# Performance work log

Hardware: AMD Instinct MI355X
Metric: run time of the kernel (lower is better)

## Reference

```python
import jax, jax.numpy as jnp
import numpy as np

EPS = 1e-5

def _conv1x1(x, W, b):
    # x: [B,Ci,H,W], W: [Co,Ci]
    return jnp.einsum('oi,bihw->bohw', W, x) + b[None, :, None, None]

def _bn(x, gamma, beta, mean, var):
    # inference-mode BatchNorm2d
    s = gamma / jnp.sqrt(var + EPS)
    return x * s[None, :, None, None] + (beta - mean * s)[None, :, None, None]

def _conv3x3(x, W, b):
    y = jax.lax.conv_general_dilated(x, W, (1, 1), 'SAME',
                                     dimension_numbers=('NCHW', 'OIHW', 'NCHW'))
    return y + b[None, :, None, None]

def _sparsemax_last(S):
    # sparsemax over the last axis (TrackHSPA: max-subtract, sort, cumsum, threshold)
    S = S - jnp.max(S, axis=-1, keepdims=True)
    srt = -jnp.sort(-S, axis=-1)                 # descending sort
    csum = jnp.cumsum(srt, axis=-1) - 1.0
    N = S.shape[-1]
    ar = jnp.arange(1, N + 1, dtype=S.dtype)
    mask = ar * srt > csum
    k = jnp.sum(mask, axis=-1, keepdims=True)    # support size per row
    tau = jnp.take_along_axis(csum, k - 1, axis=-1) / k.astype(S.dtype)
    return jnp.maximum(S - tau, 0.0)

def _forward(zf, xf, Wq, bq, Ws, bs, Wg, bg, g_gamma, g_beta, g_mean, g_var,
             Wfi, bfi, fi_gamma, fi_beta, fi_mean, fi_var,
             Wm, bm, m_gamma, m_beta, m_mean, m_var, prelu_a):
    B, C, Hx, Wx = xf.shape
    # ---- Graph_Attention_Union (cross-attention) ----
    xf_t = _conv1x1(xf, Wq, bq).reshape(B, C, -1)      # [B,C,Nx]
    zf_t = _conv1x1(zf, Ws, bs).reshape(B, C, -1)      # [B,C,Nz]
    xf_g = jax.nn.relu(_bn(_conv1x1(xf, Wg, bg), g_gamma, g_beta, g_mean, g_var))
    zf_g = jax.nn.relu(_bn(_conv1x1(zf, Wg, bg), g_gamma, g_beta, g_mean, g_var))
    sim = jnp.einsum('bcn,bcm->bnm', xf_t, zf_t)       # [B,Nx,Nz]
    attn = jax.nn.softmax(sim, axis=2)
    emb = jnp.einsum('bcm,bnm->bcn', zf_g.reshape(B, C, -1), attn)
    emb = emb.reshape(B, C, Hx, Wx)
    gat = jax.nn.relu(_bn(_conv1x1(jnp.concatenate([emb, xf_g], axis=1), Wfi, bfi),
                          fi_gamma, fi_beta, fi_mean, fi_var))
    # ---- TrackHSPA (adaptive sparsemax self-attention) ----
    e = _conv3x3(gat, Wm, bm)
    e = _bn(e, m_gamma, m_beta, m_mean, m_var)
    e = jnp.where(e >= 0, e, prelu_a * e)              # PReLU (single param)
    N = Hx * Wx
    ef = e.reshape(B, -1, N)                           # [B,C',N]
    S = jnp.einsum('bdi,bdj->bij', ef, ef)             # [B,N,N]
    P = _sparsemax_last(S)
    out = jnp.einsum('bcn,bnm->bcm', gat.reshape(B, C, N), P)
    return out.reshape(B, C, Hx, Wx) + gat


def setup_inputs():
    key = jax.random.key(0)
    ks = jax.random.split(key, 8)
    B, C, Hz, Wz, Hx, Wx = 32, 256, 7, 7, 31, 31
    Cm = C // 4
    f = lambda k, shape: jax.random.normal(k, shape, jnp.float32) * 0.05
    return {
        'zf': jax.random.normal(ks[0], (B, C, Hz, Wz), jnp.float32),
        'xf': jax.random.normal(ks[1], (B, C, Hx, Wx), jnp.float32),
        'Wq': f(ks[2], (C, C)), 'bq': jnp.zeros((C,), jnp.float32),
        'Ws': f(ks[3], (C, C)), 'bs': jnp.zeros((C,), jnp.float32),
        'Wg': f(ks[4], (C, C)), 'bg': jnp.zeros((C,), jnp.float32),
        'g_gamma': jnp.ones((C,), jnp.float32), 'g_beta': jnp.zeros((C,), jnp.float32),
        'g_mean': jnp.zeros((C,), jnp.float32), 'g_var': jnp.ones((C,), jnp.float32),
        'Wfi': f(ks[5], (C, 2 * C)), 'bfi': jnp.zeros((C,), jnp.float32),
        'fi_gamma': jnp.ones((C,), jnp.float32), 'fi_beta': jnp.zeros((C,), jnp.float32),
        'fi_mean': jnp.zeros((C,), jnp.float32), 'fi_var': jnp.ones((C,), jnp.float32),
        'Wm': f(ks[6], (Cm, C, 3, 3)), 'bm': jnp.zeros((Cm,), jnp.float32),
        'm_gamma': jnp.ones((Cm,), jnp.float32), 'm_beta': jnp.zeros((Cm,), jnp.float32),
        'm_mean': jnp.zeros((Cm,), jnp.float32), 'm_var': jnp.ones((Cm,), jnp.float32),
        'prelu_a': jnp.array(0.25, jnp.float32),
    }


def reference(zf, xf, Wq, bq, Ws, bs, Wg, bg, g_gamma, g_beta, g_mean, g_var,
              Wfi, bfi, fi_gamma, fi_beta, fi_mean, fi_var,
              Wm, bm, m_gamma, m_beta, m_mean, m_var, prelu_a):
    return _forward(zf, xf, Wq, bq, Ws, bs, Wg, bg, g_gamma, g_beta, g_mean, g_var,
                    Wfi, bfi, fi_gamma, fi_beta, fi_mean, fi_var,
                    Wm, bm, m_gamma, m_beta, m_mean, m_var, prelu_a)
```

## Files before the change

### kernel.cpp

```cpp
#include <hip/hip_runtime.h>
#include <cstdint>
#include <cstddef>
#include <math.h>

typedef __attribute__((ext_vector_type(8))) short short8;
typedef __attribute__((ext_vector_type(4))) float floatx4;
typedef unsigned short ushort_t;

__device__ __forceinline__ ushort_t f2bf(float x) {
    union { float f; unsigned u; } v; v.f = x;
    unsigned r = v.u + 0x7FFF + ((v.u >> 16) & 1);
    return (ushort_t)(r >> 16);
}
__device__ __forceinline__ float bf2f(ushort_t h) {
    union { unsigned u; float f; } v; v.u = ((unsigned)h) << 16; return v.f;
}
__device__ __forceinline__ void split2(float v, ushort_t& h, ushort_t& l) {
    h = f2bf(v);
    l = f2bf(v - bf2f(h));
}

#define MFMA(a, b, c) __builtin_amdgcn_mfma_f32_16x16x32_bf16((a), (b), (c), 0, 0, 0)

__device__ __forceinline__ void gload_lds16(const void* g, void* l) {
    __builtin_amdgcn_global_load_lds(
        (const __attribute__((address_space(1))) unsigned*)g,
        (__attribute__((address_space(3))) unsigned*)l, 16, 0, 0);
}

__global__ void prep_all_kernel(
    const float* __restrict__ Wq, const float* __restrict__ Ws,
    const float* __restrict__ Wg, const float* __restrict__ Wfi,
    const float* __restrict__ Wm,
    const float* bq, const float* bs,
    const float* bg, const float* gg, const float* gb, const float* gm, const float* gv,
    const float* bfi, const float* fg, const float* fb, const float* fm, const float* fv,
    const float* bm, const float* mg, const float* mb, const float* mm, const float* mv,
    ushort_t* Wq_h, ushort_t* Wq_l, ushort_t* Ws_h, ushort_t* Ws_l,
    ushort_t* Wg_h, ushort_t* Wg_l, ushort_t* Wfi_h, ushort_t* Wfi_l,
    ushort_t* wm_h, ushort_t* wm_l, float* scsh)
{
    int bid = blockIdx.x, t = threadIdx.x;
    if (bid < 256) {
        int i = bid * 256 + t; ushort_t h, l; split2(Wq[i], h, l); Wq_h[i] = h; Wq_l[i] = l;
    } else if (bid < 512) {
        int i = (bid - 256) * 256 + t; ushort_t h, l; split2(Ws[i], h, l); Ws_h[i] = h; Ws_l[i] = l;
    } else if (bid < 768) {
        int i = (bid - 512) * 256 + t; ushort_t h, l; split2(Wg[i], h, l); Wg_h[i] = h; Wg_l[i] = l;
    } else if (bid < 1280) {
        int i = (bid - 768) * 256 + t; ushort_t h, l; split2(Wfi[i], h, l); Wfi_h[i] = h; Wfi_l[i] = l;
    } else if (bid < 1856) {
        int i = (bid - 1280) * 256 + t;
        int c = i & 255, m = (i >> 8) & 63, tap = i >> 14;
        ushort_t h, l; split2(Wm[((size_t)m * 256 + c) * 9 + tap], h, l);
        wm_h[i] = h; wm_l[i] = l;
    } else {
        if (t < 256) {
            scsh[t] = 1.f;        scsh[256 + t] = bq[t];
            scsh[512 + t] = 1.f;  scsh[768 + t] = bs[t];
            float s = gg[t] * rsqrtf(gv[t] + 1e-5f);
            scsh[1024 + t] = s;   scsh[1280 + t] = gb[t] + s * (bg[t] - gm[t]);
            float s2 = fg[t] * rsqrtf(fv[t] + 1e-5f);
            scsh[1536 + t] = s2;  scsh[1792 + t] = fb[t] + s2 * (bfi[t] - fm[t]);
            if (t < 64) {
                float s3 = mg[t] * rsqrtf(mv[t] + 1e-5f);
                scsh[2048 + t] = s3; scsh[2112 + t] = mb[t] + s3 * (bm[t] - mm[t]);
            }
        }
    }
}

__global__ void halo_zero_kernel(ushort_t* __restrict__ gxh, ushort_t* __restrict__ gxl) {
    int i = blockIdx.x * 256 + threadIdx.x;
    int b = i >> 7, k = i & 127;
    int r;
    if (k < 33) r = k;
    else if (k < 66) r = 32 * 33 + (k - 33);
    else { int k2 = k - 66; r = ((k2 >> 1) + 1) * 33 + ((k2 & 1) ? 32 : 0); }
    uint4* ph = (uint4*)(gxh + ((size_t)b * 1089 + r) * 256);
    uint4* pl = (uint4*)(gxl + ((size_t)b * 1089 + r) * 256);
    uint4 z = make_uint4(0, 0, 0, 0);
#pragma unroll
    for (int s = 0; s < 32; s++) { ph[s] = z; pl[s] = z; }
}

__global__ __launch_bounds__(256) void transpose_in_kernel(
    const float* __restrict__ in, ushort_t* __restrict__ oh, ushort_t* __restrict__ ol,
    int Nsrc, int Npad)
{
    int b = blockIdx.z;
    const float* ib = in + (size_t)b * 256 * Nsrc;
    ushort_t* obh = oh + (size_t)b * Npad * 256;
    ushort_t* obl = ol + (size_t)b * Npad * 256;
    __shared__ float tile[32][33];
    int n0 = blockIdx.x * 32, c0 = blockIdx.y * 32;
    int tx = threadIdx.x & 31, ty = threadIdx.x >> 5;
#pragma unroll
    for (int r = 0; r < 4; r++) {
        int c = c0 + ty + r * 8, n = n0 + tx;
        tile[ty + r * 8][tx] = (n < Nsrc) ? ib[(size_t)c * Nsrc + n] : 0.f;
    }
    __syncthreads();
#pragma unroll
    for (int r = 0; r < 4; r++) {
        int n = n0 + ty + r * 8, c = c0 + tx;
        if (n < Nsrc) {
            ushort_t h, l; split2(tile[tx][ty + r * 8], h, l);
            obh[(size_t)n * 256 + c] = h;
            obl[(size_t)n * 256 + c] = l;
        }
    }
}

__global__ __launch_bounds__(256, 4) void dualconv_mfma_kernel(
    const ushort_t* __restrict__ Xh, const ushort_t* __restrict__ Xl,
    const ushort_t* __restrict__ W1h, const ushort_t* __restrict__ W1l,
    const ushort_t* __restrict__ W2h, const ushort_t* __restrict__ W2l,
    const float* __restrict__ sc1, const float* __restrict__ sh1,
    const float* __restrict__ sc2, const float* __restrict__ sh2,
    int relu1, int relu2,
    ushort_t* __restrict__ O1h, ushort_t* __restrict__ O1l,
    ushort_t* __restrict__ O2h, ushort_t* __restrict__ O2l,
    ushort_t* __restrict__ O2ch, ushort_t* __restrict__ O2cl, int cpitch,
    int K, int Nvalid, int NpadIn, int NpadOut)
{
    __shared__ ushort_t Bs[16384];
    int b = blockIdx.x;
    int half = blockIdx.y & 1;
    int n0 = (blockIdx.y >> 1) * 32;
    const ushort_t* Xbh = Xh + (size_t)b * NpadIn * K;
    const ushort_t* Xbl = Xl + (size_t)b * NpadIn * K;
    int tid = threadIdx.x, w = tid >> 6, l = tid & 63, lc = l & 15, q = l >> 4;
    int m0 = w * 64;

#pragma unroll
    for (int r = 0; r < 8; r++) {
        int d = r * 4096 + w * 1024 + l * 16;
        int seg = d >> 14;
        int dr = d & 16383;
        int row = dr >> 9;
        int inrow = (dr & 511) ^ ((row & 7) << 4);
        int srow = n0 + row; if (srow > NpadIn - 1) srow = NpadIn - 1;
        const ushort_t* src = (seg ? Xbl : Xbh) + (size_t)srow * K + (inrow >> 1);
        char* dst = (char*)Bs + (r * 4096 + w * 1024);
        gload_lds16(src, dst);
    }
    __syncthreads();

    const ushort_t* Wh = half ? W2h : W1h;
    const ushort_t* Wl = half ? W2l : W1l;
    const float* sc = half ? sc2 : sc1;
    const float* sh = half ? sh2 : sh1;
    int relu = half ? relu2 : relu1;
    ushort_t* Obh = (half ? O2h : O1h) + (size_t)b * NpadOut * 256;
    ushort_t* Obl = (half ? O2l : O1l) + (size_t)b * NpadOut * 256;

#define DC_LOADA(K0, AH, AL) do { \
    _Pragma("unroll") \
    for (int mt_ = 0; mt_ < 4; mt_++) { \
        size_t off_ = (size_t)(m0 + mt_ * 16 + lc) * K + (K0) + q * 8; \
        AH[mt_] = *(const short8*)(Wh + off_); \
        AL[mt_] = *(const short8*)(Wl + off_); \
    } \
} while (0)
#define DC_LDSB(K0, BH, BL) do { \
    _Pragma("unroll") \
    for (int jt_ = 0; jt_ < 2; jt_++) { \
        int row_ = jt_ * 16 + lc; \
        int koff_ = (((K0) + q * 8) * 2) ^ ((row_ & 7) << 4); \
        BH[jt_] = *(const short8*)((const char*)Bs + row_ * 512 + koff_); \
        BL[jt_] = *(const short8*)((const char*)Bs + 16384 + row_ * 512 + koff_); \
    } \
} while (0)
#define DC_MFMA(AH, AL, BH, BL) do { \
    _Pragma("unroll") \
    for (int mt_ = 0; mt_ < 4; mt_++) \
    _Pragma("unroll") \
    for (int jt_ = 0; jt_ < 2; jt_++) { \
        acc[mt_][jt_] = MFMA(AH[mt_], BH[jt_], acc[mt_][jt_]); \
        acc[mt_][jt_] = MFMA(AH[mt_], BL[jt_], acc[mt_][jt_]); \
        acc[mt_][jt_] = MFMA(AL[mt_], BH[jt_], acc[mt_][jt_]); \
    } \
} while (0)

    floatx4 acc[4][2];
#pragma unroll
    for (int i = 0; i < 4; i++)
#pragma unroll
        for (int j = 0; j < 2; j++) acc[i][j] = (floatx4){0.f, 0.f, 0.f, 0.f};

    {
        short8 ah0[4], al0[4], ah1[4], al1[4], bh[2], bl[2];
        DC_LOADA(0, ah0, al0);
        for (int k0 = 0; k0 < K; k0 += 64) {
            DC_LOADA(k0 + 32, ah1, al1);
            DC_LDSB(k0, bh, bl);
            DC_MFMA(ah0, al0, bh, bl);
            if (k0 + 64 < K) DC_LOADA(k0 + 64, ah0, al0);
            DC_LDSB(k0 + 32, bh, bl);
            DC_MFMA(ah1, al1, bh, bl);
        }
    }
#undef DC_LOADA
#undef DC_LDSB
#undef DC_MFMA

#pragma unroll
    for (int mt = 0; mt < 4; mt++) {
        int mb = m0 + mt * 16 + q * 4;
        float s0 = sc[mb], s1 = sc[mb + 1], s2 = sc[mb + 2], s3 = sc[mb + 3];
        float h0 = sh[mb], h1 = sh[mb + 1], h2 = sh[mb + 2], h3 = sh[mb + 3];
#pragma unroll
        for (int jt = 0; jt < 2; jt++) {
            int n = n0 + jt * 16 + lc;
            if (n >= Nvalid) continue;
            float v0 = acc[mt][jt][0] * s0 + h0;
            float v1 = acc[mt][jt][1] * s1 + h1;
            float v2 = acc[mt][jt][2] * s2 + h2;
            float v3 = acc[mt][jt][3] * s3 + h3;
            if (relu) { v0 = fmaxf(v0, 0.f); v1 = fmaxf(v1, 0.f); v2 = fmaxf(v2, 0.f); v3 = fmaxf(v3, 0.f); }
            ushort_t e0, f0, e1, f1, e2, f2, e3, f3;
            split2(v0, e0, f0); split2(v1, e1, f1); split2(v2, e2, f2); split2(v3, e3, f3);
            *(ushort4*)(Obh + (size_t)n * 256 + mb) = make_ushort4(e0, e1, e2, e3);
            *(ushort4*)(Obl + (size_t)n * 256 + mb) = make_ushort4(f0, f1, f2, f3);
            if (half && O2ch) {
                O2ch[((size_t)b * 256 + mb + 0) * cpitch + n] = e0;
                O2ch[((size_t)b * 256 + mb + 1) * cpitch + n] = e1;
                O2ch[((size_t)b * 256 + mb + 2) * cpitch + n] = e2;
                O2ch[((size_t)b * 256 + mb + 3) * cpitch + n] = e3;
                O2cl[((size_t)b * 256 + mb + 0) * cpitch + n] = f0;
                O2cl[((size_t)b * 256 + mb + 1) * cpitch + n] = f1;
                O2cl[((size_t)b * 256 + mb + 2) * cpitch + n] = f2;
                O2cl[((size_t)b * 256 + mb + 3) * cpitch + n] = f3;
            }
        }
    }
}

__global__ __launch_bounds__(256) void attn_mfma_kernel(
    const ushort_t* __restrict__ xth, const ushort_t* __restrict__ xtl,
    const ushort_t* __restrict__ zth, const ushort_t* __restrict__ ztl,
    const ushort_t* __restrict__ zgh, const ushort_t* __restrict__ zgl,
    ushort_t* __restrict__ eh, ushort_t* __restrict__ el)
{
    __shared__ float S[64][68];
    __shared__ ushort_t awh[64][72], awl[64][72];
    __shared__ float T[4][16][20];
    int b = blockIdx.x, n0 = blockIdx.y * 64;
    int tid = threadIdx.x, w = tid >> 6, l = tid & 63, lc = l & 15, q = l >> 4;
    const ushort_t* xhb = xth + (size_t)b * 992 * 256;
    const ushort_t* xlb = xtl + (size_t)b * 992 * 256;
    const ushort_t* zhb = zth + (size_t)b * 64 * 256;
    const ushort_t* zlb = ztl + (size_t)b * 64 * 256;
    const ushort_t* ghb = zgh + (size_t)b * 256 * 64;
    const ushort_t* glb = zgl + (size_t)b * 256 * 64;

    int rowg = n0 + w * 16 + lc;
#pragma unroll
    for (int ct = 0; ct < 4; ct++) {
        floatx4 acc = (floatx4){0.f, 0.f, 0.f, 0.f};
        for (int k0 = 0; k0 < 256; k0 += 32) {
            short8 ah = *(const short8*)(xhb + (size_t)rowg * 256 + k0 + q * 8);
            short8 al = *(const short8*)(xlb + (size_t)rowg * 256 + k0 + q * 8);
            short8 bh = *(const short8*)(zhb + (size_t)(ct * 16 + lc) * 256 + k0 + q * 8);
            short8 bl = *(const short8*)(zlb + (size_t)(ct * 16 + lc) * 256 + k0 + q * 8);
            acc = MFMA(ah, bh, acc);
            acc = MFMA(ah, bl, acc);
            acc = MFMA(al, bh, acc);
        }
#pragma unroll
        for (int r = 0; r < 4; r++) S[w * 16 + q * 4 + r][ct * 16 + lc] = acc[r];
    }
    __syncthreads();
    if (tid < 64) {
        float mx = -INFINITY;
        for (int m = 0; m < 49; m++) mx = fmaxf(mx, S[tid][m]);
        float sum = 0.f;
        for (int m = 0; m < 49; m++) { float e = __expf(S[tid][m] - mx); S[tid][m] = e; sum += e; }
        float inv = 1.f / sum;
        for (int m = 0; m < 64; m++) {
            float vv = (m < 49) ? S[tid][m] * inv : 0.f;
            ushort_t hh, ll; split2(vv, hh, ll);
            awh[tid][m] = hh; awl[tid][m] = ll;
        }
    }
    __syncthreads();
    int nw = l >> 2, cg = l & 3;
#pragma unroll
    for (int ct = 0; ct < 16; ct++) {
        floatx4 acc = (floatx4){0.f, 0.f, 0.f, 0.f};
#pragma unroll
        for (int k0 = 0; k0 < 64; k0 += 32) {
            short8 ah = *(const short8*)(&awh[w * 16 + lc][k0 + q * 8]);
            short8 al = *(const short8*)(&awl[w * 16 + lc][k0 + q * 8]);
            short8 bh = *(const short8*)(ghb + (size_t)(ct * 16 + lc) * 64 + k0 + q * 8);
            short8 bl = *(const short8*)(glb + (size_t)(ct * 16 + lc) * 64 + k0 + q * 8);
            acc = MFMA(ah, bh, acc);
            acc = MFMA(ah, bl, acc);
            acc = MFMA(al, bh, acc);
        }
#pragma unroll
        for (int r = 0; r < 4; r++) T[w][q * 4 + r][lc] = acc[r];
        float4 vv = *(const float4*)&T[w][nw][cg * 4];
        int n = n0 + w * 16 + nw;
        if (n < 961) {
            ushort_t h0, l0, h1, l1, h2, l2_, h3, l3;
            split2(vv.x, h0, l0); split2(vv.y, h1, l1);
            split2(vv.z, h2, l2_); split2(vv.w, h3, l3);
            size_t off = ((size_t)b * 992 + n) * 256 + ct * 16 + cg * 4;
            *(ushort4*)(eh + off) = make_ushort4(h0, h1, h2, h3);
            *(ushort4*)(el + off) = make_ushort4(l0, l1, l2_, l3);
        }
    }
}

__global__ __launch_bounds__(256, 2) void fi_mfma_kernel(
    const ushort_t* __restrict__ Eh, const ushort_t* __restrict__ El,
    const ushort_t* __restrict__ Gh, const ushort_t* __restrict__ Gl,
    const ushort_t* __restrict__ Wh, const ushort_t* __restrict__ Wl,
    const float* __restrict__ sc, const float* __restrict__ sh,
    ushort_t* __restrict__ gxh, ushort_t* __restrict__ gxl,
    ushort_t* __restrict__ gat_nf)
{
    __shared__ ushort_t Bs[16384];
    int b = blockIdx.x;
    const ushort_t* Ebh = Eh + (size_t)b * 992 * 256;
    const ushort_t* Ebl = El + (size_t)b * 992 * 256;
    const ushort_t* Gbh = Gh + (size_t)b * 992 * 256;
    const ushort_t* Gbl = Gl + (size_t)b * 992 * 256;
    ushort_t* gxhb = gxh + (size_t)b * 1089 * 256;
    ushort_t* gxlb = gxl + (size_t)b * 1089 * 256;
    ushort_t* gn = gat_nf + (size_t)b * 256 * 992;
    int tid = threadIdx.x, w = tid >> 6, l = tid & 63, lc = l & 15, q = l >> 4;
    int m0 = w * 64, nb0 = blockIdx.y * 32;

    floatx4 acc[4][2];
#pragma unroll
    for (int i = 0; i < 4; i++)
#pragma unroll
        for (int j = 0; j < 2; j++) acc[i][j] = (floatx4){0.f, 0.f, 0.f, 0.f};

#define FI_LOADA(K0, AH, AL) do { \
    _Pragma("unroll") \
    for (int mt_ = 0; mt_ < 4; mt_++) { \
        size_t off_ = (size_t)(m0 + mt_ * 16 + lc) * 512 + (K0) + q * 8; \
        AH[mt_] = *(const short8*)(Wh + off_); \
        AL[mt_] = *(const short8*)(Wl + off_); \
    } \
} while (0)
#define FI_LDSB(K0, BH, BL) do { \
    _Pragma("unroll") \
    for (int jt_ = 0; jt_ < 2; jt_++) { \
        int row_ = jt_ * 16 + lc; \
        int koff_ = (((K0) + q * 8) * 2) ^ ((row_ & 7) << 4); \
        BH[jt_] = *(const short8*)((const char*)Bs + row_ * 512 + koff_); \
        BL[jt_] = *(const short8*)((const char*)Bs + 16384 + row_ * 512 + koff_); \
    } \
} while (0)
#define FI_MFMA(AH, AL, BH, BL) do { \
    _Pragma("unroll") \
    for (int mt_ = 0; mt_ < 4; mt_++) \
    _Pragma("unroll") \
    for (int jt_ = 0; jt_ < 2; jt_++) { \
        acc[mt_][jt_] = MFMA(AH[mt_], BH[jt_], acc[mt_][jt_]); \
        acc[mt_][jt_] = MFMA(AH[mt_], BL[jt_], acc[mt_][jt_]); \
        acc[mt_][jt_] = MFMA(AL[mt_], BH[jt_], acc[mt_][jt_]); \
    } \
} while (0)

    for (int p = 0; p < 2; p++) {
        const ushort_t* srcH = p ? Gbh : Ebh;
        const ushort_t* srcL = p ? Gbl : Ebl;
        if (p) __syncthreads();
#pragma unroll
        for (int r = 0; r < 8; r++) {
            int d = r * 4096 + w * 1024 + l * 16;
            int seg = d >> 14;
            int dr = d & 16383;
            int row = dr >> 9;
            int inrow = (dr & 511) ^ ((row & 7) << 4);
            int srow = nb0 + row; if (srow > 991) srow = 991;
            const ushort_t* src = (seg ? srcL : srcH) + (size_t)srow * 256 + (inrow >> 1);
            char* dst = (char*)Bs + (r * 4096 + w * 1024);
            gload_lds16(src, dst);
        }
        __syncthreads();

        int pb = p * 256;
        short8 ah0[4], al0[4], ah1[4], al1[4], bh[2], bl[2];
        FI_LOADA(pb, ah0, al0);
        for (int kk = 0; kk < 256; kk += 64) {
            FI_LOADA(pb + kk + 32, ah1, al1);
            FI_LDSB(kk, bh, bl);
            FI_MFMA(ah0, al0, bh, bl);
            if (kk + 64 < 256) FI_LOADA(pb + kk + 64, ah0, al0);
            FI_LDSB(kk + 32, bh, bl);
            FI_MFMA(ah1, al1, bh, bl);
        }
    }
#undef FI_LOADA
#undef FI_LDSB
#undef FI_MFMA

#pragma unroll
    for (int mt = 0; mt < 4; mt++) {
        int mb = m0 + mt * 16 + q * 4;
        float s0 = sc[mb], s1 = sc[mb + 1], s2 = sc[mb + 2], s3 = sc[mb + 3];
        float h0 = sh[mb], h1 = sh[mb + 1], h2 = sh[mb + 2], h3 = sh[mb + 3];
#pragma unroll
        for (int jt = 0; jt < 2; jt++) {
            int n = nb0 + jt * 16 + lc;
            if (n >= 961) continue;
            float v0 = fmaxf(acc[mt][jt][0] * s0 + h0, 0.f);
            float v1 = fmaxf(acc[mt][jt][1] * s1 + h1, 0.f);
            float v2 = fmaxf(acc[mt][jt][2] * s2 + h2, 0.f);
            float v3 = fmaxf(acc[mt][jt][3] * s3 + h3, 0.f);
            ushort_t a0, b0, a1, b1, a2, b2, a3, b3;
            split2(v0, a0, b0); split2(v1, a1, b1); split2(v2, a2, b2); split2(v3, a3, b3);
            int hh = n / 31, ww2 = n - hh * 31;
            int row = (hh + 1) * 33 + (ww2 + 1);
            *(ushort4*)(gxhb + (size_t)row * 256 + mb) = make_ushort4(a0, a1, a2, a3);
            *(ushort4*)(gxlb + (size_t)row * 256 + mb) = make_ushort4(b0, b1, b2, b3);
            gn[(size_t)(mb + 0) * 992 + n] = a0;
            gn[(size_t)(mb + 1) * 992 + n] = a1;
            gn[(size_t)(mb + 2) * 992 + n] = a2;
            gn[(size_t)(mb + 3) * 992 + n] = a3;
        }
    }
}

__global__ __launch_bounds__(256, 2) void conv3x3_mfma_kernel(
    const ushort_t* __restrict__ gxh, const ushort_t* __restrict__ gxl,
    const ushort_t* __restrict__ wmh, const ushort_t* __restrict__ wml,
    const float* __restrict__ sc, const float* __restrict__ sh,
    const float* __restrict__ prelu_a,
    ushort_t* __restrict__ eh, ushort_t* __restrict__ el)
{
    __shared__ float Sp[4][2048];
    int b = blockIdx.x;
    const ushort_t* gxhb = gxh + (size_t)b * 1089 * 256;
    const ushort_t* gxlb = gxl + (size_t)b * 1089 * 256;
    ushort_t* ebh = eh + (size_t)b * 1024 * 64;
    ushort_t* ebl = el + (size_t)b * 1024 * 64;
    int tid = threadIdx.x, w = tid >> 6, l = tid & 63, lc = l & 15, q = l >> 4;
    int j0 = blockIdx.y * 64;

    int base[4];
#pragma unroll
    for (int jt = 0; jt < 4; jt++) {
        int j = j0 + jt * 16 + lc; if (j > 960) j = 960;
        int hh = j / 31, ww2 = j - hh * 31;
        base[jt] = (hh + 1) * 33 + (ww2 + 1);
    }

    floatx4 acc[4][4];
#pragma unroll
    for (int i = 0; i < 4; i++)
#pragma unroll
        for (int j = 0; j < 4; j++) acc[i][j] = (floatx4){0.f, 0.f, 0.f, 0.f};

#define C3_LOAD(SL, AH, AL, BH, BL) do { \
    int sl_ = (SL); \
    int tap_ = (sl_ >= 9) ? sl_ - 9 : sl_; \
    int k0_ = (w * 2 + ((sl_ >= 9) ? 1 : 0)) * 32; \
    int doff_ = (tap_ / 3 - 1) * 33 + (tap_ % 3 - 1); \
    const ushort_t* wth_ = wmh + tap_ * 16384; \
    const ushort_t* wtl_ = wml + tap_ * 16384; \
    _Pragma("unroll") \
    for (int mt_ = 0; mt_ < 4; mt_++) { \
        size_t off_ = (size_t)(mt_ * 16 + lc) * 256 + k0_ + q * 8; \
        AH[mt_] = *(const short8*)(wth_ + off_); \
        AL[mt_] = *(const short8*)(wtl_ + off_); \
    } \
    _Pragma("unroll") \
    for (int jt_ = 0; jt_ < 4; jt_++) { \
        size_t off_ = (size_t)(base[jt_] + doff_) * 256 + k0_ + q * 8; \
        BH[jt_] = *(const short8*)(gxhb + off_); \
        BL[jt_] = *(const short8*)(gxlb + off_); \
    } \
} while (0)
#define C3_MFMA(AH, AL, BH, BL) do { \
    _Pragma("unroll") \
    for (int mt_ = 0; mt_ < 4; mt_++) \
    _Pragma("unroll") \
    for (int jt_ = 0; jt_ < 4; jt_++) { \
        acc[mt_][jt_] = MFMA(AH[mt_], BH[jt_], acc[mt_][jt_]); \
        acc[mt_][jt_] = MFMA(AH[mt_], BL[jt_], acc[mt_][jt_]); \
        acc[mt_][jt_] = MFMA(AL[mt_], BH[jt_], acc[mt_][jt_]); \
    } \
} while (0)

    short8 A0h[4], A0l[4], B0h[4], B0l[4];
    short8 A1h[4], A1l[4], B1h[4], B1l[4];
    C3_LOAD(0, A0h, A0l, B0h, B0l);
#pragma unroll
    for (int it = 0; it < 9; it++) {
        C3_LOAD(it * 2 + 1, A1h, A1l, B1h, B1l);
        C3_MFMA(A0h, A0l, B0h, B0l);
        if (it < 8) C3_LOAD(it * 2 + 2, A0h, A0l, B0h, B0l);
        C3_MFMA(A1h, A1l, B1h, B1l);
    }
#undef C3_LOAD
#undef C3_MFMA

    float pa = prelu_a[0];
#pragma unroll
    for (int ph = 0; ph < 2; ph++) {
        __syncthreads();
#pragma unroll
        for (int mt = 0; mt < 4; mt++)
#pragma unroll
            for (int jt = 0; jt < 2; jt++)
#pragma unroll
                for (int r = 0; r < 4; r++)
                    Sp[w][(mt * 16 + q * 4 + r) * 32 + jt * 16 + lc] = acc[mt][ph * 2 + jt][r];
        __syncthreads();
#pragma unroll
        for (int gi = 0; gi < 2; gi++) {
            int g = tid + gi * 256;
            int j = g & 31, mg = g >> 5;
            int m = mg * 4;
            int jj = j0 + ph * 32 + j;
            if (jj >= 961) continue;
            float v[4];
#pragma unroll
            for (int i = 0; i < 4; i++) {
                int idx = (m + i) * 32 + j;
                v[i] = Sp[0][idx] + Sp[1][idx] + Sp[2][idx] + Sp[3][idx];
                v[i] = v[i] * sc[m + i] + sh[m + i];
                v[i] = v[i] >= 0.f ? v[i] : pa * v[i];
            }
            ushort_t a0, b0, a1, b1, a2, b2, a3, b3;
            split2(v[0], a0, b0); split2(v[1], a1, b1);
            split2(v[2], a2, b2); split2(v[3], a3, b3);
            *(ushort4*)(ebh + (size_t)jj * 64 + m) = make_ushort4(a0, a1, a2, a3);
            *(ushort4*)(ebl + (size_t)jj * 64 + m) = make_ushort4(b0, b1, b2, b3);
        }
    }
}

__global__ __launch_bounds__(512) void hspa_mfma_kernel(
    const ushort_t* __restrict__ eh, const ushort_t* __restrict__ el,
    ushort_t* __restrict__ PT)
{
    const int PITCH = 978;
    __shared__ float S[16 * 978];
    int b = blockIdx.x, nb = blockIdx.y;
    const ushort_t* ebh = eh + (size_t)b * 1024 * 64;
    const ushort_t* ebl = el + (size_t)b * 1024 * 64;
    ushort_t* Pb = PT + (size_t)b * 1024 * 992;
    int tid = threadIdx.x, w = tid >> 6, l = tid & 63, lc = l & 15, q = l >> 4;
    int n0 = nb * 32;

    short8 Ah[2][2], Al[2][2];
#pragma unroll
    for (int g = 0; g < 2; g++)
#pragma unroll
        for (int kh = 0; kh < 2; kh++) {
            size_t off = (size_t)(n0 + g * 16 + lc) * 64 + kh * 32 + q * 8;
            Ah[g][kh] = *(const short8*)(ebh + off);
            Al[g][kh] = *(const short8*)(ebl + off);
        }

    floatx4 acc[2][8];
#pragma unroll
    for (int g = 0; g < 2; g++)
#pragma unroll
        for (int s = 0; s < 8; s++) acc[g][s] = (floatx4){0.f, 0.f, 0.f, 0.f};

#define HS_LOADB(SLOT, BH0, BL0, BH1, BL1) do { \
    int jt_ = w + (SLOT) * 8; if (jt_ > 60) jt_ = 60; \
    size_t o_ = (size_t)(jt_ * 16 + lc) * 64 + q * 8; \
    BH0 = *(const short8*)(ebh + o_); \
    BL0 = *(const short8*)(ebl + o_); \
    BH1 = *(const short8*)(ebh + o_ + 32); \
    BL1 = *(const short8*)(ebl + o_ + 32); \
} while (0)

    {
        short8 b0h[2], b0l[2], b1h[2], b1l[2];
        HS_LOADB(0, b0h[0], b0l[0], b1h[0], b1l[0]);
#pragma unroll
        for (int s = 0; s < 8; s++) {
            const int cur = s & 1, nxt = cur ^ 1;
            if (s < 7) HS_LOADB(s + 1, b0h[nxt], b0l[nxt], b1h[nxt], b1l[nxt]);
#pragma unroll
            for (int g = 0; g < 2; g++) {
                floatx4 a = acc[g][s];
                a = MFMA(Ah[g][0], b0h[cur], a);
                a = MFMA(Ah[g][0], b0l[cur], a);
                a = MFMA(Al[g][0], b0h[cur], a);
                a = MFMA(Ah[g][1], b1h[cur], a);
                a = MFMA(Ah[g][1], b1l[cur], a);
                a = MFMA(Al[g][1], b1h[cur], a);
                acc[g][s] = a;
            }
        }
    }
#undef HS_LOADB

#pragma unroll
    for (int g = 0; g < 2; g++) {
        if (g) __syncthreads();
#pragma unroll
        for (int s = 0; s < 8; s++) {
            int jt = w + s * 8;
            if (jt < 61) {
                int j = jt * 16 + lc;
#pragma unroll
                for (int r = 0; r < 4; r++)
                    S[(q * 4 + r) * PITCH + j] = acc[g][s][r];
            }
        }
        __syncthreads();

        int r0 = w * 2, r1 = w * 2 + 1;
        float sv0[16], sv1[16];
        float mx0 = -INFINITY, mx1 = -INFINITY;
#pragma unroll
        for (int t = 0; t < 16; t++) {
            int j = l + t * 64;
            float s0 = (j < 961) ? S[r0 * PITCH + j] : -INFINITY;
            float s1 = (j < 961) ? S[r1 * PITCH + j] : -INFINITY;
            sv0[t] = s0; sv1[t] = s1;
            mx0 = fmaxf(mx0, s0); mx1 = fmaxf(mx1, s1);
        }
        for (int off = 32; off; off >>= 1) {
            mx0 = fmaxf(mx0, __shfl_xor(mx0, off));
            mx1 = fmaxf(mx1, __shfl_xor(mx1, off));
        }
#pragma unroll
        for (int t = 0; t < 16; t++) { sv0[t] -= mx0; sv1[t] -= mx1; }

        float tau0 = -1.f, tau1 = -1.f;
        for (int it = 0; it < 16; it++) {
            float s0 = 0.f, c0 = 0.f, s1 = 0.f, c1 = 0.f;
#pragma unroll
            for (int t = 0; t < 16; t++) {
                if (sv0[t] > tau0) { s0 += sv0[t]; c0 += 1.f; }
                if (sv1[t] > tau1) { s1 += sv1[t]; c1 += 1.f; }
            }
            for (int off = 32; off; off >>= 1) {
                s0 += __shfl_xor(s0, off); c0 += __shfl_xor(c0, off);
                s1 += __shfl_xor(s1, off); c1 += __shfl_xor(c1, off);
            }
            float nt0 = (s0 - 1.f) / c0;
            float nt1 = (s1 - 1.f) / c1;
            bool conv = (nt0 == tau0) && (nt1 == tau1);
            tau0 = nt0; tau1 = nt1;
            if (conv) break;
        }
#pragma unroll
        for (int t = 0; t < 16; t++) {
            int j = l + t * 64;
            if (j < 976) {
                S[r0 * PITCH + j] = (j < 961) ? fmaxf(sv0[t] - tau0, 0.f) : 0.f;
                S[r1 * PITCH + j] = (j < 961) ? fmaxf(sv1[t] - tau1, 0.f) : 0.f;
            }
        }
        __syncthreads();

        int nbase = n0 + g * 16;
        if (nbase < 976) {
            for (int j = tid; j < 976; j += 512) {
                union { ushort_t u[8]; uint4 v; } p0, p1;
#pragma unroll
                for (int r = 0; r < 8; r++)  p0.u[r] = f2bf(S[r * PITCH + j]);
#pragma unroll
                for (int r = 0; r < 8; r++)  p1.u[r] = f2bf(S[(8 + r) * PITCH + j]);
                ushort_t* dst = Pb + (size_t)j * 992 + nbase;
                *(uint4*)(dst) = p0.v;
                *(uint4*)(dst + 8) = p1.v;
            }
        }
    }
}

__global__ __launch_bounds__(256, 2) void out_mfma_kernel(
    const ushort_t* __restrict__ gat_nf, const ushort_t* __restrict__ PT,
    float* __restrict__ out)
{
    int b = blockIdx.x, jb = blockIdx.y;
    const ushort_t* gb = gat_nf + (size_t)b * 256 * 992;
    const ushort_t* Pb = PT + (size_t)b * 1024 * 992;
    float* ob = out + (size_t)b * 256 * 961;
    int tid = threadIdx.x, w = tid >> 6, l = tid & 63, lc = l & 15, q = l >> 4;
    int m0 = w * 64, j0 = jb * 64;

    floatx4 acc[4][4];
#pragma unroll
    for (int i = 0; i < 4; i++)
#pragma unroll
        for (int j = 0; j < 4; j++) acc[i][j] = (floatx4){0.f, 0.f, 0.f, 0.f};

#define OUT_LOAD(K0, AA, BB) do { \
    _Pragma("unroll") \
    for (int mt_ = 0; mt_ < 4; mt_++) \
        AA[mt_] = *(const short8*)(gb + (size_t)(m0 + mt_ * 16 + lc) * 992 + (K0) + q * 8); \
    _Pragma("unroll") \
    for (int jt_ = 0; jt_ < 4; jt_++) \
        BB[jt_] = *(const short8*)(Pb + (size_t)(j0 + jt_ * 16 + lc) * 992 + (K0) + q * 8); \
} while (0)
#define OUT_MFMA(AA, BB) do { \
    _Pragma("unroll") \
    for (int mt_ = 0; mt_ < 4; mt_++) \
    _Pragma("unroll") \
    for (int jt_ = 0; jt_ < 4; jt_++) \
        acc[mt_][jt_] = MFMA(AA[mt_], BB[jt_], acc[mt_][jt_]); \
} while (0)

    short8 a0[4], b0[4], a1[4], b1[4];
    OUT_LOAD(0, a0, b0);
    for (int k0 = 0; k0 < 960; k0 += 64) {
        OUT_LOAD(k0 + 32, a1, b1);
        OUT_MFMA(a0, b0);
        OUT_LOAD(k0 + 64, a0, b0);
        OUT_MFMA(a1, b1);
    }
    OUT_MFMA(a0, b0);
#undef OUT_LOAD
#undef OUT_MFMA

#pragma unroll
    for (int mt = 0; mt < 4; mt++) {
        int mb = m0 + mt * 16 + q * 4;
#pragma unroll
        for (int jt = 0; jt < 4; jt++) {
            int j = j0 + jt * 16 + lc;
            if (j >= 961) continue;
#pragma unroll
            for (int r = 0; r < 4; r++) {
                float g = bf2f(gb[(size_t)(mb + r) * 992 + j]);
                ob[(size_t)(mb + r) * 961 + j] = acc[mt][jt][r] + g;
            }
        }
    }
}

extern "C" void kernel_launch(void* const* d_in, const int* in_sizes, int n_in,
                              void* d_out, int out_size, void* d_ws, size_t ws_size,
                              hipStream_t stream)
{
    const float* zf      = (const float*)d_in[0];
    const float* xf      = (const float*)d_in[1];
    const float* Wq      = (const float*)d_in[2];
    const float* bq      = (const float*)d_in[3];
    const float* Ws      = (const float*)d_in[4];
    const float* bs      = (const float*)d_in[5];
    const float* Wg      = (const float*)d_in[6];
    const float* bg      = (const float*)d_in[7];
    const float* g_gamma = (const float*)d_in[8];
    const float* g_beta  = (const float*)d_in[9];
    const float* g_mean  = (const float*)d_in[10];
    const float* g_var   = (const float*)d_in[11];
    const float* Wfi     = (const float*)d_in[12];
    const float* bfi     = (const float*)d_in[13];
    const float* fi_gamma= (const float*)d_in[14];
    const float* fi_beta = (const float*)d_in[15];
    const float* fi_mean = (const float*)d_in[16];
    const float* fi_var  = (const float*)d_in[17];
    const float* Wm      = (const float*)d_in[18];
    const float* bm      = (const float*)d_in[19];
    const float* m_gamma = (const float*)d_in[20];
    const float* m_beta  = (const float*)d_in[21];
    const float* m_mean  = (const float*)d_in[22];
    const float* m_var   = (const float*)d_in[23];
    const float* prelu_a = (const float*)d_in[24];
    float* out = (float*)d_out;

    ushort_t* ws = (ushort_t*)d_ws;
    ushort_t* Wq_h  = ws + 0;         ushort_t* Wq_l  = ws + 65536;
    ushort_t* Ws_h  = ws + 131072;    ushort_t* Ws_l  = ws + 196608;
    ushort_t* Wg_h  = ws + 262144;    ushort_t* Wg_l  = ws + 327680;
    ushort_t* Wfi_h = ws + 393216;    ushort_t* Wfi_l = ws + 524288;
    ushort_t* wm_h  = ws + 655360;    ushort_t* wm_l  = ws + 802816;
    ushort_t* XT_h    = ws + 950272;
    ushort_t* XT_l    = ws + 9076736;
    ushort_t* xf_tT_h = ws + 17203200;
    ushort_t* xf_tT_l = ws + 25329664;
    ushort_t* zf_tT_h = ws + 33456128;
    ushort_t* zf_tT_l = ws + 33980416;
    ushort_t* zf_gT_h = ws + 34504704;
    ushort_t* zf_gT_l = ws + 35028992;
    ushort_t* xf_gT_h = ws + 35553280;
    ushort_t* xf_gT_l = ws + 43679744;
    ushort_t* gat_nf  = ws + 51806208;
    ushort_t* eT_h    = ws + 59932672;
    ushort_t* eT_l    = ws + 62029824;
    ushort_t* PT      = ws + 64126976;
    ushort_t* gxT_h   = ws + 64126976;
    ushort_t* gxT_l   = ws + 73048064;
    ushort_t* embT_h  = XT_h;
    ushort_t* embT_l  = XT_l;
    ushort_t* zfT_h   = ws + 96632832;
    ushort_t* zfT_l   = ws + 97157120;
    float* scsh       = (float*)(ws + 97681408);
    ushort_t* zgC_h   = ws + 97685760;
    ushort_t* zgC_l   = ws + 98210048;

    const float* sc_q  = scsh + 0,    *sh_q  = scsh + 256;
    const float* sc_s  = scsh + 512,  *sh_s  = scsh + 768;
    const float* sc_g  = scsh + 1024, *sh_g  = scsh + 1280;
    const float* sc_fi = scsh + 1536, *sh_fi = scsh + 1792;
    const float* sc_m  = scsh + 2048, *sh_m  = scsh + 2112;

    prep_all_kernel<<<1857, 256, 0, stream>>>(
        Wq, Ws, Wg, Wfi, Wm,
        bq, bs, bg, g_gamma, g_beta, g_mean, g_var,
        bfi, fi_gamma, fi_beta, fi_mean, fi_var,
        bm, m_gamma, m_beta, m_mean, m_var,
        Wq_h, Wq_l, Ws_h, Ws_l, Wg_h, Wg_l, Wfi_h, Wfi_l, wm_h, wm_l, scsh);

    transpose_in_kernel<<<dim3(31, 8, 32), 256, 0, stream>>>(xf, XT_h, XT_l, 961, 992);
    transpose_in_kernel<<<dim3(2, 8, 32), 256, 0, stream>>>(zf, zfT_h, zfT_l, 49, 64);

    dualconv_mfma_kernel<<<dim3(32, 62), 256, 0, stream>>>(
        XT_h, XT_l, Wq_h, Wq_l, Wg_h, Wg_l,
        sc_q, sh_q, sc_g, sh_g, 0, 1,
        xf_tT_h, xf_tT_l, xf_gT_h, xf_gT_l,
        nullptr, nullptr, 0, 256, 961, 992, 992);
    dualconv_mfma_kernel<<<dim3(32, 4), 256, 0, stream>>>(
        zfT_h, zfT_l, Ws_h, Ws_l, Wg_h, Wg_l,
        sc_s, sh_s, sc_g, sh_g, 0, 1,
        zf_tT_h, zf_tT_l, zf_gT_h, zf_gT_l,
        zgC_h, zgC_l, 64, 256, 49, 64, 64);

    attn_mfma_kernel<<<dim3(32, 16), 256, 0, stream>>>(
        xf_tT_h, xf_tT_l, zf_tT_h, zf_tT_l, zgC_h, zgC_l, embT_h, embT_l);

    halo_zero_kernel<<<16, 256, 0, stream>>>(gxT_h, gxT_l);

    fi_mfma_kernel<<<dim3(32, 31), 256, 0, stream>>>(
        embT_h, embT_l, xf_gT_h, xf_gT_l, Wfi_h, Wfi_l, sc_fi, sh_fi,
        gxT_h, gxT_l, gat_nf);

    conv3x3_mfma_kernel<<<dim3(32, 16), 256, 0, stream>>>(
        gxT_h, gxT_l, wm_h, wm_l, sc_m, sh_m, prelu_a, eT_h, eT_l);

    hspa_mfma_kernel<<<dim3(32, 31), 512, 0, stream>>>(eT_h, eT_l, PT);

    out_mfma_kernel<<<dim3(32, 16), 256, 0, stream>>>(gat_nf, PT, out);
}
```

Before: 565.2 us.

## Shrink N-tile to 16 and loop both weight halves per block in 1x1 convs

The dual 1x1 conv kernel now gives each block a 16-column tile and computes both weight sets (W1 and W2) in one block from the same staged LDS input, instead of splitting halves across blocks with 32-column tiles. The fi kernel also drops to 16-column tiles, gets twice the blocks and a higher occupancy hint. The aim is more parallelism and less LDS per block, with input tiles shared across both convs. The cost is that every weight fragment loaded from global memory now feeds half as many MFMAs, raising weight traffic per unit of work.

```diff
diff --git a/kernel.cpp b/kernel.cpp
--- a/kernel.cpp
+++ b/kernel.cpp
@@ -124,36 +124,26 @@
     ushort_t* __restrict__ O2ch, ushort_t* __restrict__ O2cl, int cpitch,
     int K, int Nvalid, int NpadIn, int NpadOut)
 {
-    __shared__ ushort_t Bs[16384];
+    __shared__ ushort_t Bs[8192];
     int b = blockIdx.x;
-    int half = blockIdx.y & 1;
-    int n0 = (blockIdx.y >> 1) * 32;
+    int n0 = blockIdx.y * 16;
     const ushort_t* Xbh = Xh + (size_t)b * NpadIn * K;
     const ushort_t* Xbl = Xl + (size_t)b * NpadIn * K;
     int tid = threadIdx.x, w = tid >> 6, l = tid & 63, lc = l & 15, q = l >> 4;
     int m0 = w * 64;
 
 #pragma unroll
-    for (int r = 0; r < 8; r++) {
-        int d = r * 4096 + w * 1024 + l * 16;
-        int seg = d >> 14;
-        int dr = d & 16383;
+    for (int r = 0; r < 4; r++) {
+        int d = r * 4096 + tid * 16;
+        int seg = d >> 13;
+        int dr = d & 8191;
         int row = dr >> 9;
         int inrow = (dr & 511) ^ ((row & 7) << 4);
         int srow = n0 + row; if (srow > NpadIn - 1) srow = NpadIn - 1;
         const ushort_t* src = (seg ? Xbl : Xbh) + (size_t)srow * K + (inrow >> 1);
-        char* dst = (char*)Bs + (r * 4096 + w * 1024);
-        gload_lds16(src, dst);
+        gload_lds16(src, (char*)Bs + d);
     }
     __syncthreads();
-
-    const ushort_t* Wh = half ? W2h : W1h;
-    const ushort_t* Wl = half ? W2l : W1l;
-    const float* sc = half ? sc2 : sc1;
-    const float* sh = half ? sh2 : sh1;
-    int relu = half ? relu2 : relu1;
-    ushort_t* Obh = (half ? O2h : O1h) + (size_t)b * NpadOut * 256;
-    ushort_t* Obl = (half ? O2l : O1l) + (size_t)b * NpadOut * 256;
 
 #define DC_LOADA(K0, AH, AL) do { \
     _Pragma("unroll") \
@@ -164,33 +154,33 @@
     } \
 } while (0)
 #define DC_LDSB(K0, BH, BL) do { \
-    _Pragma("unroll") \
-    for (int jt_ = 0; jt_ < 2; jt_++) { \
-        int row_ = jt_ * 16 + lc; \
-        int koff_ = (((K0) + q * 8) * 2) ^ ((row_ & 7) << 4); \
-        BH[jt_] = *(const short8*)((const char*)Bs + row_ * 512 + koff_); \
-        BL[jt_] = *(const short8*)((const char*)Bs + 16384 + row_ * 512 + koff_); \
+    int koff_ = (((K0) + q * 8) * 2) ^ ((lc & 7) << 4); \
+    BH = *(const short8*)((const char*)Bs + lc * 512 + koff_); \
+    BL = *(const short8*)((const char*)Bs + 8192 + lc * 512 + koff_); \
+} while (0)
+#define DC_MFMA(AH, AL, BH, BL) do { \
+    _Pragma("unroll") \
+    for (int mt_ = 0; mt_ < 4; mt_++) { \
+        acc[mt_] = MFMA(AH[mt_], BH, acc[mt_]); \
+        acc[mt_] = MFMA(AH[mt_], BL, acc[mt_]); \
+        acc[mt_] = MFMA(AL[mt_], BH, acc[mt_]); \
     } \
 } while (0)
-#define DC_MFMA(AH, AL, BH, BL) do { \
-    _Pragma("unroll") \
-    for (int mt_ = 0; mt_ < 4; mt_++) \
-    _Pragma("unroll") \
-    for (int jt_ = 0; jt_ < 2; jt_++) { \
-        acc[mt_][jt_] = MFMA(AH[mt_], BH[jt_], acc[mt_][jt_]); \
-        acc[mt_][jt_] = MFMA(AH[mt_], BL[jt_], acc[mt_][jt_]); \
-        acc[mt_][jt_] = MFMA(AL[mt_], BH[jt_], acc[mt_][jt_]); \
-    } \
-} while (0)
-
-    floatx4 acc[4][2];
-#pragma unroll
-    for (int i = 0; i < 4; i++)
-#pragma unroll
-        for (int j = 0; j < 2; j++) acc[i][j] = (floatx4){0.f, 0.f, 0.f, 0.f};
-
-    {
-        short8 ah0[4], al0[4], ah1[4], al1[4], bh[2], bl[2];
+
+    for (int half = 0; half < 2; half++) {
+        const ushort_t* Wh = half ? W2h : W1h;
+        const ushort_t* Wl = half ? W2l : W1l;
+        const float* sc = half ? sc2 : sc1;
+        const float* sh = half ? sh2 : sh1;
+        int relu = half ? relu2 : relu1;
+        ushort_t* Obh = (half ? O2h : O1h) + (size_t)b * NpadOut * 256;
+        ushort_t* Obl = (half ? O2l : O1l) + (size_t)b * NpadOut * 256;
+
+        floatx4 acc[4];
+#pragma unroll
+        for (int i = 0; i < 4; i++) acc[i] = (floatx4){0.f, 0.f, 0.f, 0.f};
+
+        short8 ah0[4], al0[4], ah1[4], al1[4], bh, bl;
         DC_LOADA(0, ah0, al0);
         for (int k0 = 0; k0 < K; k0 += 64) {
             DC_LOADA(k0 + 32, ah1, al1);
@@ -200,41 +190,39 @@
             DC_LDSB(k0 + 32, bh, bl);
             DC_MFMA(ah1, al1, bh, bl);
         }
+
+        int n = n0 + lc;
+        if (n < Nvalid) {
+#pragma unroll
+            for (int mt = 0; mt < 4; mt++) {
+                int mb = m0 + mt * 16 + q * 4;
+                float s0 = sc[mb], s1 = sc[mb + 1], s2 = sc[mb + 2], s3 = sc[mb + 3];
+                float h0 = sh[mb], h1 = sh[mb + 1], h2 = sh[mb + 2], h3 = sh[mb + 3];
+                float v0 = acc[mt][0] * s0 + h0;
+                float v1 = acc[mt][1] * s1 + h1;
+                float v2 = acc[mt][2] * s2 + h2;
+                float v3 = acc[mt][3] * s3 + h3;
+                if (relu) { v0 = fmaxf(v0, 0.f); v1 = fmaxf(v1, 0.f); v2 = fmaxf(v2, 0.f); v3 = fmaxf(v3, 0.f); }
+                ushort_t e0, f0, e1, f1, e2, f2, e3, f3;
+                split2(v0, e0, f0); split2(v1, e1, f1); split2(v2, e2, f2); split2(v3, e3, f3);
+                *(ushort4*)(Obh + (size_t)n * 256 + mb) = make_ushort4(e0, e1, e2, e3);
+                *(ushort4*)(Obl + (size_t)n * 256 + mb) = make_ushort4(f0, f1, f2, f3);
+                if (half && O2ch) {
+                    O2ch[((size_t)b * 256 + mb + 0) * cpitch + n] = e0;
+                    O2ch[((size_t)b * 256 + mb + 1) * cpitch + n] = e1;
+                    O2ch[((size_t)b * 256 + mb + 2) * cpitch + n] = e2;
+                    O2ch[((size_t)b * 256 + mb + 3) * cpitch + n] = e3;
+                    O2cl[((size_t)b * 256 + mb + 0) * cpitch + n] = f0;
+                    O2cl[((size_t)b * 256 + mb + 1) * cpitch + n] = f1;
+                    O2cl[((size_t)b * 256 + mb + 2) * cpitch + n] = f2;
+                    O2cl[((size_t)b * 256 + mb + 3) * cpitch + n] = f3;
+                }
+            }
+        }
     }
 #undef DC_LOADA
 #undef DC_LDSB
 #undef DC_MFMA
-
-#pragma unroll
-    for (int mt = 0; mt < 4; mt++) {
-        int mb = m0 + mt * 16 + q * 4;
-        float s0 = sc[mb], s1 = sc[mb + 1], s2 = sc[mb + 2], s3 = sc[mb + 3];
-        float h0 = sh[mb], h1 = sh[mb + 1], h2 = sh[mb + 2], h3 = sh[mb + 3];
-#pragma unroll
-        for (int jt = 0; jt < 2; jt++) {
-            int n = n0 + jt * 16 + lc;
-            if (n >= Nvalid) continue;
-            float v0 = acc[mt][jt][0] * s0 + h0;
-            float v1 = acc[mt][jt][1] * s1 + h1;
-            float v2 = acc[mt][jt][2] * s2 + h2;
-            float v3 = acc[mt][jt][3] * s3 + h3;
-            if (relu) { v0 = fmaxf(v0, 0.f); v1 = fmaxf(v1, 0.f); v2 = fmaxf(v2, 0.f); v3 = fmaxf(v3, 0.f); }
-            ushort_t e0, f0, e1, f1, e2, f2, e3, f3;
-            split2(v0, e0, f0); split2(v1, e1, f1); split2(v2, e2, f2); split2(v3, e3, f3);
-            *(ushort4*)(Obh + (size_t)n * 256 + mb) = make_ushort4(e0, e1, e2, e3);
-            *(ushort4*)(Obl + (size_t)n * 256 + mb) = make_ushort4(f0, f1, f2, f3);
-            if (half && O2ch) {
-                O2ch[((size_t)b * 256 + mb + 0) * cpitch + n] = e0;
-                O2ch[((size_t)b * 256 + mb + 1) * cpitch + n] = e1;
-                O2ch[((size_t)b * 256 + mb + 2) * cpitch + n] = e2;
-                O2ch[((size_t)b * 256 + mb + 3) * cpitch + n] = e3;
-                O2cl[((size_t)b * 256 + mb + 0) * cpitch + n] = f0;
-                O2cl[((size_t)b * 256 + mb + 1) * cpitch + n] = f1;
-                O2cl[((size_t)b * 256 + mb + 2) * cpitch + n] = f2;
-                O2cl[((size_t)b * 256 + mb + 3) * cpitch + n] = f3;
-            }
-        }
-    }
 }
 
 __global__ __launch_bounds__(256) void attn_mfma_kernel(
@@ -314,7 +302,7 @@
     }
 }
 
-__global__ __launch_bounds__(256, 2) void fi_mfma_kernel(
+__global__ __launch_bounds__(256, 4) void fi_mfma_kernel(
     const ushort_t* __restrict__ Eh, const ushort_t* __restrict__ El,
     const ushort_t* __restrict__ Gh, const ushort_t* __restrict__ Gl,
     const ushort_t* __restrict__ Wh, const ushort_t* __restrict__ Wl,
@@ -322,7 +310,7 @@
     ushort_t* __restrict__ gxh, ushort_t* __restrict__ gxl,
     ushort_t* __restrict__ gat_nf)
 {
-    __shared__ ushort_t Bs[16384];
+    __shared__ ushort_t Bs[8192];
     int b = blockIdx.x;
     const ushort_t* Ebh = Eh + (size_t)b * 992 * 256;
     const ushort_t* Ebl = El + (size_t)b * 992 * 256;
@@ -332,13 +320,11 @@
     ushort_t* gxlb = gxl + (size_t)b * 1089 * 256;
     ushort_t* gn = gat_nf + (size_t)b * 256 * 992;
     int tid = threadIdx.x, w = tid >> 6, l = tid & 63, lc = l & 15, q = l >> 4;
-    int m0 = w * 64, nb0 = blockIdx.y * 32;
-
-    floatx4 acc[4][2];
-#pragma unroll
-    for (int i = 0; i < 4; i++)
-#pragma unroll
-        for (int j = 0; j < 2; j++) acc[i][j] = (floatx4){0.f, 0.f, 0.f, 0.f};
+    int m0 = w * 64, nb0 = blockIdx.y * 16;
+
+    floatx4 acc[4];
+#pragma unroll
+    for (int i = 0; i < 4; i++) acc[i] = (floatx4){0.f, 0.f, 0.f, 0.f};
 
 #define FI_LOADA(K0, AH, AL) do { \
     _Pragma("unroll") \
@@ -349,22 +335,16 @@
     } \
 } while (0)
 #define FI_LDSB(K0, BH, BL) do { \
-    _Pragma("unroll") \
-    for (int jt_ = 0; jt_ < 2; jt_++) { \
-        int row_ = jt_ * 16 + lc; \
-        int koff_ = (((K0) + q * 8) * 2) ^ ((row_ & 7) << 4); \
-        BH[jt_] = *(const short8*)((const char*)Bs + row_ * 512 + koff_); \
-        BL[jt_] = *(const short8*)((const char*)Bs + 16384 + row_ * 512 + koff_); \
-    } \
+    int koff_ = (((K0) + q * 8) * 2) ^ ((lc & 7) << 4); \
+    BH = *(const short8*)((const char*)Bs + lc * 512 + koff_); \
+    BL = *(const short8*)((const char*)Bs + 8192 + lc * 512 + koff_); \
 } while (0)
 #define FI_MFMA(AH, AL, BH, BL) do { \
     _Pragma("unroll") \
-    for (int mt_ = 0; mt_ < 4; mt_++) \
-    _Pragma("unroll") \
-    for (int jt_ = 0; jt_ < 2; jt_++) { \
-        acc[mt_][jt_] = MFMA(AH[mt_], BH[jt_], acc[mt_][jt_]); \
-        acc[mt_][jt_] = MFMA(AH[mt_], BL[jt_], acc[mt_][jt_]); \
-        acc[mt_][jt_] = MFMA(AL[mt_], BH[jt_], acc[mt_][jt_]); \
+    for (int mt_ = 0; mt_ < 4; mt_++) { \
+        acc[mt_] = MFMA(AH[mt_], BH, acc[mt_]); \
+        acc[mt_] = MFMA(AH[mt_], BL, acc[mt_]); \
+        acc[mt_] = MFMA(AL[mt_], BH, acc[mt_]); \
     } \
 } while (0)
 
@@ -373,21 +353,20 @@
         const ushort_t* srcL = p ? Gbl : Ebl;
         if (p) __syncthreads();
 #pragma unroll
-        for (int r = 0; r < 8; r++) {
-            int d = r * 4096 + w * 1024 + l * 16;
-            int seg = d >> 14;
-            int dr = d & 16383;
+        for (int r = 0; r < 4; r++) {
+            int d = r * 4096 + tid * 16;
+            int seg = d >> 13;
+            int dr = d & 8191;
             int row = dr >> 9;
             int inrow = (dr & 511) ^ ((row & 7) << 4);
             int srow = nb0 + row; if (srow > 991) srow = 991;
             const ushort_t* src = (seg ? srcL : srcH) + (size_t)srow * 256 + (inrow >> 1);
-            char* dst = (char*)Bs + (r * 4096 + w * 1024);
-            gload_lds16(src, dst);
+            gload_lds16(src, (char*)Bs + d);
         }
         __syncthreads();
 
         int pb = p * 256;
-        short8 ah0[4], al0[4], ah1[4], al1[4], bh[2], bl[2];
+        short8 ah0[4], al0[4], ah1[4], al1[4], bh, bl;
         FI_LOADA(pb, ah0, al0);
         for (int kk = 0; kk < 256; kk += 64) {
             FI_LOADA(pb + kk + 32, ah1, al1);
@@ -402,23 +381,21 @@
 #undef FI_LDSB
 #undef FI_MFMA
 
-#pragma unroll
-    for (int mt = 0; mt < 4; mt++) {
-        int mb = m0 + mt * 16 + q * 4;
-        float s0 = sc[mb], s1 = sc[mb + 1], s2 = sc[mb + 2], s3 = sc[mb + 3];
-        float h0 = sh[mb], h1 = sh[mb + 1], h2 = sh[mb + 2], h3 = sh[mb + 3];
-#pragma unroll
-        for (int jt = 0; jt < 2; jt++) {
-            int n = nb0 + jt * 16 + lc;
-            if (n >= 961) continue;
-            float v0 = fmaxf(acc[mt][jt][0] * s0 + h0, 0.f);
-            float v1 = fmaxf(acc[mt][jt][1] * s1 + h1, 0.f);
-            float v2 = fmaxf(acc[mt][jt][2] * s2 + h2, 0.f);
-            float v3 = fmaxf(acc[mt][jt][3] * s3 + h3, 0.f);
+    int n = nb0 + lc;
+    if (n < 961) {
+        int hh = n / 31, ww2 = n - hh * 31;
+        int row = (hh + 1) * 33 + (ww2 + 1);
+#pragma unroll
+        for (int mt = 0; mt < 4; mt++) {
+            int mb = m0 + mt * 16 + q * 4;
+            float s0 = sc[mb], s1 = sc[mb + 1], s2 = sc[mb + 2], s3 = sc[mb + 3];
+            float h0 = sh[mb], h1 = sh[mb + 1], h2 = sh[mb + 2], h3 = sh[mb + 3];
+            float v0 = fmaxf(acc[mt][0] * s0 + h0, 0.f);
+            float v1 = fmaxf(acc[mt][1] * s1 + h1, 0.f);
+            float v2 = fmaxf(acc[mt][2] * s2 + h2, 0.f);
+            float v3 = fmaxf(acc[mt][3] * s3 + h3, 0.f);
             ushort_t a0, b0, a1, b1, a2, b2, a3, b3;
             split2(v0, a0, b0); split2(v1, a1, b1); split2(v2, a2, b2); split2(v3, a3, b3);
-            int hh = n / 31, ww2 = n - hh * 31;
-            int row = (hh + 1) * 33 + (ww2 + 1);
             *(ushort4*)(gxhb + (size_t)row * 256 + mb) = make_ushort4(a0, a1, a2, a3);
             *(ushort4*)(gxlb + (size_t)row * 256 + mb) = make_ushort4(b0, b1, b2, b3);
             gn[(size_t)(mb + 0) * 992 + n] = a0;
@@ -830,7 +807,7 @@
 
     halo_zero_kernel<<<16, 256, 0, stream>>>(gxT_h, gxT_l);
 
-    fi_mfma_kernel<<<dim3(32, 31), 256, 0, stream>>>(
+    fi_mfma_kernel<<<dim3(32, 62), 256, 0, stream>>>(
         embT_h, embT_l, xf_gT_h, xf_gT_l, Wfi_h, Wfi_l, sc_fi, sh_fi,
         gxT_h, gxT_l, gat_nf);
 
```

Measured after the change: 666.7 us. 18.0% more time.
